# Optimization experiments

Hardware: AMD Instinct MI355X
Metric: run time of the kernel (lower is better)

## Reference

```python
import jax, jax.numpy as jnp
import numpy as np

NUM_EMBEDDINGS = 1024
EMBEDDING_DIM = 256
COMMITMENT_COST = 0.25


def setup_inputs() -> dict:
    key = jax.random.key(0)
    k1, k2 = jax.random.split(key)
    inputs = jax.random.normal(k1, (32, EMBEDDING_DIM, 32, 32), dtype=jnp.float32)
    # codebook init matches torch: uniform(-1/K, 1/K)
    weight = jax.random.uniform(
        k2, (NUM_EMBEDDINGS, EMBEDDING_DIM), dtype=jnp.float32,
        minval=-1.0 / NUM_EMBEDDINGS, maxval=1.0 / NUM_EMBEDDINGS)
    return {"inputs": inputs, "weight": weight}


def reference(inputs, weight):
    # inputs: [B, C, H, W] with C == EMBEDDING_DIM; weight: [K, D]
    x = jnp.transpose(inputs, (0, 2, 3, 1))            # [B, H, W, D]
    input_shape = x.shape
    flat = x.reshape(-1, EMBEDDING_DIM)                # [N, D]

    distances = (jnp.sum(flat * flat, axis=1, keepdims=True)
                 + jnp.sum(weight * weight, axis=1)
                 - 2.0 * (flat @ weight.T))
    encoding_indices = jnp.argmin(distances, axis=1)   # [N]
    encodings = jax.nn.one_hot(encoding_indices, NUM_EMBEDDINGS, dtype=jnp.float32)  # [N, K]

    # one_hot @ weight == gather; use gather for efficiency (same values)
    quantized = weight[encoding_indices].reshape(input_shape)  # [B, H, W, D]

    e_latent_loss = jnp.mean((jax.lax.stop_gradient(quantized) - x) ** 2)
    q_latent_loss = jnp.mean((quantized - jax.lax.stop_gradient(x)) ** 2)
    loss = q_latent_loss + COMMITMENT_COST * e_latent_loss

    # straight-through estimator
    quantized_st = x + jax.lax.stop_gradient(quantized - x)

    avg_probs = jnp.mean(encodings, axis=0)            # [K]
    perplexity = jnp.exp(-jnp.sum(avg_probs * jnp.log(avg_probs + 1e-10)))

    return (loss,
            jnp.transpose(quantized_st, (0, 3, 1, 2)),  # back to [B, C, H, W]
            perplexity,
            encodings)
```

## Files before the change

### kernel.cpp

```cpp
#include <hip/hip_runtime.h>
#include <hip/hip_bf16.h>

#define HWDIM 1024
#define DDIM 256
#define KCODES 1024
#define NROWS 32768
#define BSTRIDE (DDIM * HWDIM)
#define GUARD 1.5e-4f
#define APAD 520

typedef __attribute__((ext_vector_type(8))) short short8;
typedef __attribute__((ext_vector_type(4))) float f32x4;
typedef unsigned long long ull;


__device__ __forceinline__ unsigned short f2bf(float v) {
  __hip_bfloat16 b = __float2bfloat16(v);
  return *reinterpret_cast<unsigned short*>(&b);
}
__device__ __forceinline__ float bf2f(unsigned short u) {
  __hip_bfloat16 b;
  *reinterpret_cast<unsigned short*>(&b) = u;
  return __bfloat162float(b);
}
__device__ __forceinline__ ull pk(float d, int k) {
  unsigned ub = __float_as_uint(d);
  ub = (ub & 0x80000000u) ? ~ub : (ub | 0x80000000u);
  return ((ull)ub << 32) | (unsigned)k;
}
__device__ __forceinline__ float keyq(ull key) {
  unsigned ub = (unsigned)(key >> 32);
  unsigned orig = (ub & 0x80000000u) ? (ub & 0x7FFFFFFFu) : ~ub;
  return __uint_as_float(orig);
}
__device__ __forceinline__ float keyq32(unsigned ub) {
  unsigned orig = (ub & 0x80000000u) ? (ub & 0x7FFFFFFFu) : ~ub;
  return __uint_as_float(orig);
}

__device__ __forceinline__ float pair128_sq(const float* p, int stride) {
  float a[8];
#pragma unroll
  for (int j = 0; j < 8; ++j) { float v = p[j * stride]; a[j] = __fmul_rn(v, v); }
  for (int i = 8; i < 128; i += 8) {
#pragma unroll
    for (int j = 0; j < 8; ++j) {
      float v = p[(i + j) * stride];
      a[j] = __fadd_rn(a[j], __fmul_rn(v, v));
    }
  }
  float s01 = __fadd_rn(a[0], a[1]), s23 = __fadd_rn(a[2], a[3]);
  float s45 = __fadd_rn(a[4], a[5]), s67 = __fadd_rn(a[6], a[7]);
  return __fadd_rn(__fadd_rn(s01, s23), __fadd_rn(s45, s67));
}

__global__ __launch_bounds__(256) void k_prep(
    const float* __restrict__ w, float* __restrict__ wT, float* __restrict__ ss,
    int* __restrict__ hist, double* __restrict__ loss,
    int* __restrict__ wcount, int* __restrict__ pcount,
    unsigned short* __restrict__ wh8, unsigned short* __restrict__ wl8) {
  __shared__ float tile[64][65];
  const int t = threadIdx.x;
  int g = blockIdx.x * 256 + t;
  {
    int k = g >> 5, oct = g & 31;
    const float* p = w + k * DDIM + oct * 8;
    short8 hv, lv;
#pragma unroll
    for (int j = 0; j < 8; ++j) {
      float v = p[j];
      unsigned short h = f2bf(v);
      unsigned short l = f2bf(__fsub_rn(v, bf2f(h)));
      hv[j] = (short)h; lv[j] = (short)l;
    }
    *(short8*)&wh8[oct * 8192 + k * 8] = hv;
    *(short8*)&wl8[oct * 8192 + k * 8] = lv;
  }
  if (g < KCODES) {
    hist[g] = 0;
    const float* p = w + g * DDIM;
    ss[g] = __fadd_rn(pair128_sq(p, 1), pair128_sq(p + 128, 1));
  }
  if (g == 0) { *loss = 0.0; *wcount = 0; *pcount = 0; }
  if (blockIdx.x < 64) {
    const int k0 = (blockIdx.x & 15) * 64, d0 = (blockIdx.x >> 4) * 64;
    const int c = t & 63, r = t >> 6;
#pragma unroll
    for (int m = 0; m < 16; ++m)
      tile[r + m * 4][c] = w[(k0 + r + m * 4) * DDIM + d0 + c];
    __syncthreads();
#pragma unroll
    for (int m = 0; m < 16; ++m)
      wT[(size_t)(d0 + r + m * 4) * KCODES + k0 + c] = tile[c][r + m * 4];
  }
}

__global__ __launch_bounds__(256, 1) void k_argmfma(
    const float* __restrict__ in,
    const unsigned short* __restrict__ wh8, const unsigned short* __restrict__ wl8,
    const float* __restrict__ ss, unsigned* __restrict__ kkarr,
    int* __restrict__ wlist, int* __restrict__ wcount,
    int* __restrict__ plist, int* __restrict__ pcount) {
  __shared__ __align__(16) unsigned short Ah[32 * APAD];
  __shared__ __align__(16) unsigned short Al[32 * APAD];
  __shared__ __align__(16) float ss_l[1024];
  __shared__ ull best1[64], best2[64];
  __shared__ unsigned best3[64];

  const int t = threadIdx.x;
  const int n0 = blockIdx.x * 64;
  const int b = n0 >> 10, hw0 = n0 & 1023;

  const int wv = t >> 6, ln = t & 63;
  const int cw = wv * 64;
  const int l15 = ln & 15, quad = ln >> 4;

  {
    const int hw = t & 63, dg = t >> 6;
    const float* xp = in + b * BSTRIDE + hw0 + hw;
#pragma unroll
    for (int dd = 0; dd < 64; dd += 2) {
      int d = dg * 64 + dd;
      float f0 = __builtin_nontemporal_load(&xp[d * HWDIM]);
      float f1 = __builtin_nontemporal_load(&xp[(d + 1) * HWDIM]);
      unsigned short h0 = f2bf(f0);
      unsigned short l0 = f2bf(__fsub_rn(f0, bf2f(h0)));
      unsigned short h1 = f2bf(f1);
      unsigned short l1 = f2bf(__fsub_rn(f1, bf2f(h1)));
      int base = (d >> 3) * APAD + hw * 8 + (d & 7);
      *(unsigned*)&Ah[base] = (unsigned)h0 | ((unsigned)h1 << 16);
      *(unsigned*)&Al[base] = (unsigned)l0 | ((unsigned)l1 << 16);
    }
  }
  *(float4*)&ss_l[t * 4] = *(const float4*)&ss[t * 4];
  if (t < 64) { best1[t] = ~0ull; best2[t] = ~0ull; best3[t] = 0xFFFFFFFFu; }
  __syncthreads();

  ull rb1[16], rb2[16];
  unsigned rb3[16];
#pragma unroll
  for (int i = 0; i < 16; ++i) { rb1[i] = ~0ull; rb2[i] = ~0ull; rb3[i] = 0xFFFFFFFFu; }

  for (int kb = 0; kb < 4; ++kb) {
    const int cb = kb * 256 + cw;
    f32x4 acc[4][4];
#pragma unroll
    for (int rt = 0; rt < 4; ++rt)
#pragma unroll
      for (int ct = 0; ct < 4; ++ct) acc[rt][ct] = (f32x4){0.f, 0.f, 0.f, 0.f};

#pragma unroll
    for (int ki = 0; ki < 8; ++ki) {
      const int obase = ki * 4 + quad;
      short8 ah[4], al[4], bh[4], bl[4];
#pragma unroll
      for (int rt = 0; rt < 4; ++rt) {
        int row = rt * 16 + l15;
        ah[rt] = *(const short8*)&Ah[obase * APAD + row * 8];
        al[rt] = *(const short8*)&Al[obase * APAD + row * 8];
      }
#pragma unroll
      for (int ct = 0; ct < 4; ++ct) {
        int off = obase * 8192 + (cb + ct * 16 + l15) * 8;
        bh[ct] = *(const short8*)&wh8[off];
        bl[ct] = *(const short8*)&wl8[off];
      }
      __builtin_amdgcn_s_setprio(1);
#pragma unroll
      for (int rt = 0; rt < 4; ++rt)
#pragma unroll
        for (int ct = 0; ct < 4; ++ct) {
          acc[rt][ct] = __builtin_amdgcn_mfma_f32_16x16x32_bf16(ah[rt], bh[ct], acc[rt][ct], 0, 0, 0);
          acc[rt][ct] = __builtin_amdgcn_mfma_f32_16x16x32_bf16(ah[rt], bl[ct], acc[rt][ct], 0, 0, 0);
          acc[rt][ct] = __builtin_amdgcn_mfma_f32_16x16x32_bf16(al[rt], bh[ct], acc[rt][ct], 0, 0, 0);
        }
      __builtin_amdgcn_s_setprio(0);
    }

    float sv[4];
#pragma unroll
    for (int ct = 0; ct < 4; ++ct) sv[ct] = ss_l[cb + ct * 16 + l15];
#pragma unroll
    for (int rt = 0; rt < 4; ++rt)
#pragma unroll
      for (int reg = 0; reg < 4; ++reg) {
        int idx = rt * 4 + reg;
        ull b1 = rb1[idx], b2 = rb2[idx];
        unsigned b3 = rb3[idx];
#pragma unroll
        for (int ct = 0; ct < 4; ++ct) {
          float q = fmaf(-2.f, acc[rt][ct][reg], sv[ct]);
          ull key = pk(q, cb + ct * 16 + l15);
          unsigned k32 = (unsigned)(key >> 32);
          if (key < b1)      { b3 = (unsigned)(b2 >> 32); b2 = b1; b1 = key; }
          else if (key < b2) { b3 = (unsigned)(b2 >> 32); b2 = key; }
          else if (k32 < b3) { b3 = k32; }
        }
        rb1[idx] = b1; rb2[idx] = b2; rb3[idx] = b3;
      }
  }

#pragma unroll
  for (int rt = 0; rt < 4; ++rt)
#pragma unroll
    for (int reg = 0; reg < 4; ++reg)
      atomicMin(&best1[rt * 16 + quad * 4 + reg], rb1[rt * 4 + reg]);
  __syncthreads();
#pragma unroll
  for (int rt = 0; rt < 4; ++rt)
#pragma unroll
    for (int reg = 0; reg < 4; ++reg) {
      int row = rt * 16 + quad * 4 + reg;
      int idx = rt * 4 + reg;
      ull sub = (rb1[idx] == best1[row]) ? rb2[idx] : rb1[idx];
      atomicMin(&best2[row], sub);
    }
  __syncthreads();
#pragma unroll
  for (int rt = 0; rt < 4; ++rt)
#pragma unroll
    for (int reg = 0; reg < 4; ++reg) {
      int row = rt * 16 + quad * 4 + reg;
      int idx = rt * 4 + reg;
      ull b1 = best1[row], b2 = best2[row];
      unsigned c = (rb1[idx] != b1 && rb1[idx] != b2) ? (unsigned)(rb1[idx] >> 32)
                 : ((rb2[idx] != b1 && rb2[idx] != b2) ? (unsigned)(rb2[idx] >> 32)
                                                       : rb3[idx]);
      atomicMin(&best3[row], c);
    }
  __syncthreads();
  if (t < 64) {
    ull k1 = best1[t];
    kkarr[n0 + t] = (unsigned)(k1 & 0xFFFFFFFFull);
    float q1 = keyq(k1);
    if (!(keyq(best2[t]) - q1 > GUARD)) {
      if (keyq32(best3[t]) - q1 > GUARD) {
        int p = atomicAdd(pcount, 1);
        plist[p] = (n0 + t) | ((int)(best2[t] & 0xFFFFFFFFull) << 16);
      } else {
        int p = atomicAdd(wcount, 1);
        wlist[p] = n0 + t;
      }
    }
  }
}

__global__ __launch_bounds__(256) void k_fallback(
    const float* __restrict__ in, const float* __restrict__ w,
    const float* __restrict__ wT, const float* __restrict__ ss,
    const int* __restrict__ wlist, const int* __restrict__ wcount,
    const int* __restrict__ plist, const int* __restrict__ pcount,
    unsigned* __restrict__ kkarr) {
  __shared__ float xrow[256];
  __shared__ float rsh;
  __shared__ ull bmin;
  __shared__ ull pkeys[2];
  const int t = threadIdx.x;

  const int pc = *pcount;
  for (int i = blockIdx.x; i < pc; i += gridDim.x) {
    const int pe = plist[i];
    const int n = pe & 0xFFFF;
    const unsigned k2 = ((unsigned)pe) >> 16;
    const unsigned k1 = kkarr[n];
    const int b = n >> 10, hw = n & 1023;
    xrow[t] = in[b * BSTRIDE + t * HWDIM + hw];
    __syncthreads();
    if (t == 0) rsh = __fadd_rn(pair128_sq(xrow, 1), pair128_sq(xrow + 128, 1));
    __syncthreads();
    if (t < 2) {
      unsigned k = t ? k2 : k1;
      const float* wr = w + (size_t)k * DDIM;
      float m = 0.f;
      for (int d = 0; d < 256; ++d) m = fmaf(xrow[d], wr[d], m);
      float dist = fmaf(-2.f, m, __fadd_rn(rsh, ss[k]));
      pkeys[t] = pk(dist, (int)k);
    }
    __syncthreads();
    if (t == 0) {
      ull kmin = pkeys[0] < pkeys[1] ? pkeys[0] : pkeys[1];
      kkarr[n] = (unsigned)(kmin & 0xFFFFFFFFull);
    }
    __syncthreads();
  }

  const int cnt = *wcount;
  for (int i = blockIdx.x; i < cnt; i += gridDim.x) {
    const int n = wlist[i];
    const int b = n >> 10, hw = n & 1023;
    xrow[t] = in[b * BSTRIDE + t * HWDIM + hw];
    if (t == 0) bmin = ~0ull;
    __syncthreads();
    if (t == 0) rsh = __fadd_rn(pair128_sq(xrow, 1), pair128_sq(xrow + 128, 1));
    __syncthreads();
    float m[4] = {0.f, 0.f, 0.f, 0.f};
    for (int d = 0; d < 256; ++d) {
      float xv = xrow[d];
      const float* wd = wT + (size_t)d * KCODES + t;
      m[0] = fmaf(xv, wd[0], m[0]);
      m[1] = fmaf(xv, wd[256], m[1]);
      m[2] = fmaf(xv, wd[512], m[2]);
      m[3] = fmaf(xv, wd[768], m[3]);
    }
    ull lb = ~0ull;
#pragma unroll
    for (int j = 0; j < 4; ++j) {
      int k = t + j * 256;
      float dist = fmaf(-2.f, m[j], __fadd_rn(rsh, ss[k]));
      ull key = pk(dist, k);
      if (key < lb) lb = key;
    }
    atomicMin(&bmin, lb);
    __syncthreads();
    if (t == 0) kkarr[n] = (unsigned)(bmin & 0xFFFFFFFFull);
    __syncthreads();
  }
}

__global__ __launch_bounds__(256) void k_quantenc(
    const float* __restrict__ in, const float* __restrict__ w,
    const unsigned* __restrict__ kkarr, int* __restrict__ hist,
    float* __restrict__ enc, float* __restrict__ outq, double* __restrict__ loss) {
  __shared__ float wrow[64][65];
  __shared__ unsigned kk[64];
  __shared__ double red[256];

  const int t = threadIdx.x;
  const int q = blockIdx.x & 3;
  const int n0 = (blockIdx.x >> 2) * 64;
  const int dc = q * 64;
  const int c0 = q * 256;
  const int b = n0 >> 10, hw0 = n0 & 1023;

  if (t < 64) kk[t] = kkarr[n0 + t];
  __syncthreads();

  if (q == 0 && t < 64) atomicAdd(&hist[kk[t]], 1);

#pragma unroll 4
  for (int m = 0; m < 32; ++m) {
    int u = m * 256 + t;
    int r = u >> 7, c2 = u & 127;
    int cbase = c0 + c2 * 2;
    unsigned kr = kk[r];
    float2 v;
    v.x = (cbase == (int)kr) ? 1.0f : 0.0f;
    v.y = (cbase + 1 == (int)kr) ? 1.0f : 0.0f;
    *(float2*)&enc[(size_t)(n0 + r) * 1024 + cbase] = v;
  }

#pragma unroll
  for (int m = 0; m < 16; ++m) {
    int u = t + m * 256;
    int r = u >> 6, dd = u & 63;
    wrow[r][dd] = w[kk[r] * DDIM + dc + dd];
  }
  __syncthreads();

  const float* inb = in + b * BSTRIDE + hw0;
  float* outb = outq + b * BSTRIDE + hw0;
  const int hwl = t & 63, dl = t >> 6;
  double lsum = 0.0;
#pragma unroll
  for (int dd = 0; dd < 64; dd += 4) {
    int d = dc + dd + dl;
    float x = inb[d * HWDIM + hwl];
    float wv = wrow[hwl][dd + dl];
    float diff = __fsub_rn(wv, x);
    outb[d * HWDIM + hwl] = __fadd_rn(x, diff);
    lsum += (double)diff * (double)diff;
  }
  red[t] = lsum;
  __syncthreads();
  for (int s = 128; s > 0; s >>= 1) {
    if (t < s) red[t] += red[t + s];
    __syncthreads();
  }
  if (t == 0) atomicAdd(loss, red[0]);
}

__global__ void k_final(const int* __restrict__ hist, const double* __restrict__ loss,
                        float* __restrict__ out) {
  __shared__ double red[256];
  int t = threadIdx.x;
  double s = 0.0;
  for (int i = t; i < KCODES; i += 256) {
    double p = (double)hist[i] * (1.0 / 32768.0);
    s += p * log(p + 1e-10);
  }
  red[t] = s;
  __syncthreads();
  for (int st = 128; st > 0; st >>= 1) {
    if (t < st) red[t] += red[t + st];
    __syncthreads();
  }
  if (t == 0) {
    out[8388609] = (float)exp(-red[0]);
    double m = *loss / 8388608.0;
    out[0] = (float)(1.25 * m);
  }
}

extern "C" void kernel_launch(void* const* d_in, const int* in_sizes, int n_in,
                              void* d_out, int out_size, void* d_ws, size_t ws_size,
                              hipStream_t stream) {
  const float* in = (const float*)d_in[0];
  const float* w  = (const float*)d_in[1];
  float* out = (float*)d_out;

  char* wsb = (char*)d_ws;
  float*    wT     = (float*)   (wsb + 0);
  float*    ssp    = (float*)   (wsb + 1048576);
  unsigned* kkarr  = (unsigned*)(wsb + 1052672);
  int*      wlist  = (int*)     (wsb + 1183744);
  int*      hist   = (int*)     (wsb + 1314816);
  int*      plist  = (int*)     (wsb + 1318912);
  double*   loss   = (double*)  (wsb + 1449984);
  int*      wcount = (int*)     (wsb + 1449992);
  int*      pcount = (int*)     (wsb + 1449996);

  char* ob = (char*)d_out + 33554448;
  unsigned short* wh8 = (unsigned short*)(ob + 0);
  unsigned short* wl8 = (unsigned short*)(ob + 524288);
  float* encp = out + 8388610;

  k_prep<<<dim3(128), dim3(256), 0, stream>>>(w, wT, ssp, hist, loss, wcount, pcount, wh8, wl8);
  k_argmfma<<<dim3(512), dim3(256), 0, stream>>>(in, wh8, wl8, ssp, kkarr,
                                                 wlist, wcount, plist, pcount);
  k_fallback<<<dim3(1024), dim3(256), 0, stream>>>(in, w, wT, ssp, wlist, wcount,
                                                   plist, pcount, kkarr);
  k_quantenc<<<dim3(2048), dim3(256), 0, stream>>>(in, w, kkarr, hist, encp,
                                                   out + 1, loss);
  k_final<<<dim3(1), dim3(256), 0, stream>>>(hist, loss, out);
}
```

Baseline: 348.3 us.

## Split input bf16 hi/lo conversion into separate pre-pass kernel with MFMA-ready layout

Adds a k_split kernel that converts the fp32 NCHW input into bf16 hi/lo halves, stored in global scratch (inside the output buffer) in an octet-major layout matching the MFMA operand order. k_argmfma then loads these with contiguous 16-byte vector loads instead of doing strided fp32 loads and conversion itself, and drops the padded LDS layout. This is meant to cut the strided load latency from the single-block-per-CU GEMM kernel. In exchange it adds an extra kernel launch and a full write and re-read of about 32 MB of intermediate data, and the unpadded LDS layout may cause bank conflicts.

Result: slower. 365.1 us (+4.8%).

```diff
diff --git a/kernel.cpp b/kernel.cpp
--- a/kernel.cpp
+++ b/kernel.cpp
@@ -7,7 +7,6 @@
 #define NROWS 32768
 #define BSTRIDE (DDIM * HWDIM)
 #define GUARD 1.5e-4f
-#define APAD 520
 
 typedef __attribute__((ext_vector_type(8))) short short8;
 typedef __attribute__((ext_vector_type(4))) float f32x4;
@@ -95,41 +94,81 @@
   }
 }
 
+__global__ __launch_bounds__(256) void k_split(
+    const float* __restrict__ in,
+    unsigned short* __restrict__ AhG, unsigned short* __restrict__ AlG) {
+  __shared__ unsigned short sh[64 * 64];
+  __shared__ unsigned short sl[64 * 64];
+  const int t = threadIdx.x;
+  const int n0 = (blockIdx.x >> 2) * 64;
+  const int d0 = (blockIdx.x & 3) * 64;
+  const int b = n0 >> 10, hw0 = n0 & 1023;
+
+  {
+    const int hw = t & 63, dq = t >> 6;
+    const float* xp = in + b * BSTRIDE + hw0 + hw;
+#pragma unroll
+    for (int dd = 0; dd < 16; ++dd) {
+      int dl = dq * 16 + dd;
+      float v = xp[(d0 + dl) * HWDIM];
+      unsigned short h = f2bf(v);
+      unsigned short l = f2bf(__fsub_rn(v, bf2f(h)));
+      sh[dl * 64 + hw] = h;
+      sl[dl * 64 + hw] = l;
+    }
+  }
+  __syncthreads();
+  {
+    const int row = t & 63, oi = t >> 6;
+#pragma unroll
+    for (int it = 0; it < 2; ++it) {
+      int ol = oi + 4 * it;
+      int oct = (d0 >> 3) + ol;
+      short8 hv, lv;
+#pragma unroll
+      for (int j = 0; j < 8; ++j) {
+        hv[j] = (short)sh[(ol * 8 + j) * 64 + row];
+        lv[j] = (short)sl[(ol * 8 + j) * 64 + row];
+      }
+      size_t go = ((size_t)oct * NROWS + n0 + row) * 8;
+      *(short8*)&AhG[go] = hv;
+      *(short8*)&AlG[go] = lv;
+    }
+  }
+}
+
 __global__ __launch_bounds__(256, 1) void k_argmfma(
-    const float* __restrict__ in,
+    const unsigned short* __restrict__ AhG, const unsigned short* __restrict__ AlG,
     const unsigned short* __restrict__ wh8, const unsigned short* __restrict__ wl8,
     const float* __restrict__ ss, unsigned* __restrict__ kkarr,
     int* __restrict__ wlist, int* __restrict__ wcount,
     int* __restrict__ plist, int* __restrict__ pcount) {
-  __shared__ __align__(16) unsigned short Ah[32 * APAD];
-  __shared__ __align__(16) unsigned short Al[32 * APAD];
+  __shared__ __align__(16) unsigned short Ah[32 * 64 * 8];
+  __shared__ __align__(16) unsigned short Al[32 * 64 * 8];
   __shared__ __align__(16) float ss_l[1024];
   __shared__ ull best1[64], best2[64];
   __shared__ unsigned best3[64];
 
   const int t = threadIdx.x;
   const int n0 = blockIdx.x * 64;
-  const int b = n0 >> 10, hw0 = n0 & 1023;
-
   const int wv = t >> 6, ln = t & 63;
   const int cw = wv * 64;
   const int l15 = ln & 15, quad = ln >> 4;
 
   {
-    const int hw = t & 63, dg = t >> 6;
-    const float* xp = in + b * BSTRIDE + hw0 + hw;
-#pragma unroll
-    for (int dd = 0; dd < 64; dd += 2) {
-      int d = dg * 64 + dd;
-      float f0 = __builtin_nontemporal_load(&xp[d * HWDIM]);
-      float f1 = __builtin_nontemporal_load(&xp[(d + 1) * HWDIM]);
-      unsigned short h0 = f2bf(f0);
-      unsigned short l0 = f2bf(__fsub_rn(f0, bf2f(h0)));
-      unsigned short h1 = f2bf(f1);
-      unsigned short l1 = f2bf(__fsub_rn(f1, bf2f(h1)));
-      int base = (d >> 3) * APAD + hw * 8 + (d & 7);
-      *(unsigned*)&Ah[base] = (unsigned)h0 | ((unsigned)h1 << 16);
-      *(unsigned*)&Al[base] = (unsigned)l0 | ((unsigned)l1 << 16);
+    short8 th[8], tl[8];
+#pragma unroll
+    for (int i = 0; i < 8; ++i) {
+      int u = i * 256 + t;
+      size_t go = ((size_t)(u >> 6) * NROWS + n0 + (u & 63)) * 8;
+      th[i] = *(const short8*)&AhG[go];
+      tl[i] = *(const short8*)&AlG[go];
+    }
+#pragma unroll
+    for (int i = 0; i < 8; ++i) {
+      int u = i * 256 + t;
+      *(short8*)&Ah[u * 8] = th[i];
+      *(short8*)&Al[u * 8] = tl[i];
     }
   }
   *(float4*)&ss_l[t * 4] = *(const float4*)&ss[t * 4];
@@ -156,8 +195,8 @@
 #pragma unroll
       for (int rt = 0; rt < 4; ++rt) {
         int row = rt * 16 + l15;
-        ah[rt] = *(const short8*)&Ah[obase * APAD + row * 8];
-        al[rt] = *(const short8*)&Al[obase * APAD + row * 8];
+        ah[rt] = *(const short8*)&Ah[(obase * 64 + row) * 8];
+        al[rt] = *(const short8*)&Al[(obase * 64 + row) * 8];
       }
 #pragma unroll
       for (int ct = 0; ct < 4; ++ct) {
@@ -422,10 +461,13 @@
   char* ob = (char*)d_out + 33554448;
   unsigned short* wh8 = (unsigned short*)(ob + 0);
   unsigned short* wl8 = (unsigned short*)(ob + 524288);
+  unsigned short* AhG = (unsigned short*)(ob + 1048576);
+  unsigned short* AlG = (unsigned short*)(ob + 17825792);
   float* encp = out + 8388610;
 
   k_prep<<<dim3(128), dim3(256), 0, stream>>>(w, wT, ssp, hist, loss, wcount, pcount, wh8, wl8);
-  k_argmfma<<<dim3(512), dim3(256), 0, stream>>>(in, wh8, wl8, ssp, kkarr,
+  k_split<<<dim3(2048), dim3(256), 0, stream>>>(in, AhG, AlG);
+  k_argmfma<<<dim3(512), dim3(256), 0, stream>>>(AhG, AlG, wh8, wl8, ssp, kkarr,
                                                  wlist, wcount, plist, pcount);
   k_fallback<<<dim3(1024), dim3(256), 0, stream>>>(in, w, wT, ssp, wlist, wcount,
                                                    plist, pcount, kkarr);
```

## Stage codebook tiles in double-buffered LDS with register-resident A fragments

Applied to the files above, without the earlier changes.

The distance-argmin kernel now processes 128 rows per 512-thread block. Each wave keeps its 16-row A fragments in registers, and all waves share codebook B tiles staged through a double-buffered 128KB LDS region, prefetched from global memory one step ahead. Previously every wave loaded B fragments directly from global/L2 and re-read A from LDS. The aim is to reduce redundant global traffic and overlap loads with MFMA work. The cost is a sync per step, high LDS use that limits occupancy to one block per CU despite the launch bound of 2, and only 256 blocks.

Measured after the change: 314.9 us. 9.6% less time.

```diff
diff --git a/kernel.cpp b/kernel.cpp
--- a/kernel.cpp
+++ b/kernel.cpp
@@ -7,7 +7,6 @@
 #define NROWS 32768
 #define BSTRIDE (DDIM * HWDIM)
 #define GUARD 1.5e-4f
-#define APAD 520
 
 typedef __attribute__((ext_vector_type(8))) short short8;
 typedef __attribute__((ext_vector_type(4))) float f32x4;
@@ -95,28 +94,30 @@
   }
 }
 
-__global__ __launch_bounds__(256, 1) void k_argmfma(
+__global__ __launch_bounds__(512, 2) void k_argmfma(
     const float* __restrict__ in,
     const unsigned short* __restrict__ wh8, const unsigned short* __restrict__ wl8,
     const float* __restrict__ ss, unsigned* __restrict__ kkarr,
     int* __restrict__ wlist, int* __restrict__ wcount,
     int* __restrict__ plist, int* __restrict__ pcount) {
-  __shared__ __align__(16) unsigned short Ah[32 * APAD];
-  __shared__ __align__(16) unsigned short Al[32 * APAD];
+  __shared__ __align__(16) char smem[131072];
   __shared__ __align__(16) float ss_l[1024];
-  __shared__ ull best1[64], best2[64];
-  __shared__ unsigned best3[64];
+  __shared__ ull best1[128], best2[128];
+  __shared__ unsigned best3[128];
 
   const int t = threadIdx.x;
-  const int n0 = blockIdx.x * 64;
+  const int n0 = blockIdx.x * 128;
   const int b = n0 >> 10, hw0 = n0 & 1023;
 
   const int wv = t >> 6, ln = t & 63;
-  const int cw = wv * 64;
+  const int rw = wv * 16;
   const int l15 = ln & 15, quad = ln >> 4;
 
+  unsigned short* Ah = (unsigned short*)smem;
+  unsigned short* Al = (unsigned short*)(smem + 65536);
+
   {
-    const int hw = t & 63, dg = t >> 6;
+    const int hw = t & 127, dg = t >> 7;
     const float* xp = in + b * BSTRIDE + hw0 + hw;
 #pragma unroll
     for (int dd = 0; dd < 64; dd += 2) {
@@ -127,109 +128,146 @@
       unsigned short l0 = f2bf(__fsub_rn(f0, bf2f(h0)));
       unsigned short h1 = f2bf(f1);
       unsigned short l1 = f2bf(__fsub_rn(f1, bf2f(h1)));
-      int base = (d >> 3) * APAD + hw * 8 + (d & 7);
+      int base = ((d >> 3) * 128 + hw) * 8 + (d & 7);
       *(unsigned*)&Ah[base] = (unsigned)h0 | ((unsigned)h1 << 16);
       *(unsigned*)&Al[base] = (unsigned)l0 | ((unsigned)l1 << 16);
     }
   }
-  *(float4*)&ss_l[t * 4] = *(const float4*)&ss[t * 4];
-  if (t < 64) { best1[t] = ~0ull; best2[t] = ~0ull; best3[t] = 0xFFFFFFFFu; }
-  __syncthreads();
-
-  ull rb1[16], rb2[16];
-  unsigned rb3[16];
-#pragma unroll
-  for (int i = 0; i < 16; ++i) { rb1[i] = ~0ull; rb2[i] = ~0ull; rb3[i] = 0xFFFFFFFFu; }
-
-  for (int kb = 0; kb < 4; ++kb) {
-    const int cb = kb * 256 + cw;
-    f32x4 acc[4][4];
-#pragma unroll
-    for (int rt = 0; rt < 4; ++rt)
-#pragma unroll
-      for (int ct = 0; ct < 4; ++ct) acc[rt][ct] = (f32x4){0.f, 0.f, 0.f, 0.f};
+  *(float2*)&ss_l[t * 2] = *(const float2*)&ss[t * 2];
+  if (t < 128) { best1[t] = ~0ull; best2[t] = ~0ull; best3[t] = 0xFFFFFFFFu; }
+  __syncthreads();
+
+  short8 afh[8], afl[8];
+  {
+    const int row = rw + l15;
+#pragma unroll
+    for (int ki = 0; ki < 8; ++ki) {
+      int obase = ki * 4 + quad;
+      afh[ki] = *(const short8*)&Ah[(obase * 128 + row) * 8];
+      afl[ki] = *(const short8*)&Al[(obase * 128 + row) * 8];
+    }
+  }
+  short8 s0h[4], s0l[4];
+#pragma unroll
+  for (int j = 0; j < 4; ++j) {
+    int u = j * 512 + t;
+    int ob = u >> 6, c = u & 63;
+    s0h[j] = *(const short8*)&wh8[ob * 8192 + c * 8];
+    s0l[j] = *(const short8*)&wl8[ob * 8192 + c * 8];
+  }
+  __syncthreads();
+
+  {
+    unsigned short* Bh0 = (unsigned short*)smem;
+    unsigned short* Bl0 = (unsigned short*)(smem + 32768);
+#pragma unroll
+    for (int j = 0; j < 4; ++j) {
+      int u = j * 512 + t;
+      *(short8*)&Bh0[u * 8] = s0h[j];
+      *(short8*)&Bl0[u * 8] = s0l[j];
+    }
+  }
+  __syncthreads();
+
+  ull rb1[4], rb2[4];
+  unsigned rb3[4];
+#pragma unroll
+  for (int i = 0; i < 4; ++i) { rb1[i] = ~0ull; rb2[i] = ~0ull; rb3[i] = 0xFFFFFFFFu; }
+
+  int cur = 0;
+  for (int s = 0; s < 16; ++s) {
+    const int cb = s * 64;
+    short8 sh_[4], sl_[4];
+    if (s < 15) {
+      const int cb1 = cb + 64;
+#pragma unroll
+      for (int j = 0; j < 4; ++j) {
+        int u = j * 512 + t;
+        int ob = u >> 6, c = u & 63;
+        sh_[j] = *(const short8*)&wh8[ob * 8192 + (cb1 + c) * 8];
+        sl_[j] = *(const short8*)&wl8[ob * 8192 + (cb1 + c) * 8];
+      }
+    }
+
+    const unsigned short* Bh = (const unsigned short*)(smem + cur * 65536);
+    const unsigned short* Bl = (const unsigned short*)(smem + cur * 65536 + 32768);
+    f32x4 acc[4];
+#pragma unroll
+    for (int ct = 0; ct < 4; ++ct) acc[ct] = (f32x4){0.f, 0.f, 0.f, 0.f};
 
 #pragma unroll
     for (int ki = 0; ki < 8; ++ki) {
       const int obase = ki * 4 + quad;
-      short8 ah[4], al[4], bh[4], bl[4];
-#pragma unroll
-      for (int rt = 0; rt < 4; ++rt) {
-        int row = rt * 16 + l15;
-        ah[rt] = *(const short8*)&Ah[obase * APAD + row * 8];
-        al[rt] = *(const short8*)&Al[obase * APAD + row * 8];
-      }
+      short8 bh[4], bl[4];
 #pragma unroll
       for (int ct = 0; ct < 4; ++ct) {
-        int off = obase * 8192 + (cb + ct * 16 + l15) * 8;
-        bh[ct] = *(const short8*)&wh8[off];
-        bl[ct] = *(const short8*)&wl8[off];
-      }
-      __builtin_amdgcn_s_setprio(1);
-#pragma unroll
-      for (int rt = 0; rt < 4; ++rt)
-#pragma unroll
-        for (int ct = 0; ct < 4; ++ct) {
-          acc[rt][ct] = __builtin_amdgcn_mfma_f32_16x16x32_bf16(ah[rt], bh[ct], acc[rt][ct], 0, 0, 0);
-          acc[rt][ct] = __builtin_amdgcn_mfma_f32_16x16x32_bf16(ah[rt], bl[ct], acc[rt][ct], 0, 0, 0);
-          acc[rt][ct] = __builtin_amdgcn_mfma_f32_16x16x32_bf16(al[rt], bh[ct], acc[rt][ct], 0, 0, 0);
-        }
-      __builtin_amdgcn_s_setprio(0);
+        int uo = (obase * 64 + ct * 16 + l15) * 8;
+        bh[ct] = *(const short8*)&Bh[uo];
+        bl[ct] = *(const short8*)&Bl[uo];
+      }
+#pragma unroll
+      for (int ct = 0; ct < 4; ++ct) {
+        acc[ct] = __builtin_amdgcn_mfma_f32_16x16x32_bf16(afh[ki], bh[ct], acc[ct], 0, 0, 0);
+        acc[ct] = __builtin_amdgcn_mfma_f32_16x16x32_bf16(afh[ki], bl[ct], acc[ct], 0, 0, 0);
+        acc[ct] = __builtin_amdgcn_mfma_f32_16x16x32_bf16(afl[ki], bh[ct], acc[ct], 0, 0, 0);
+      }
     }
 
     float sv[4];
 #pragma unroll
     for (int ct = 0; ct < 4; ++ct) sv[ct] = ss_l[cb + ct * 16 + l15];
 #pragma unroll
-    for (int rt = 0; rt < 4; ++rt)
-#pragma unroll
-      for (int reg = 0; reg < 4; ++reg) {
-        int idx = rt * 4 + reg;
-        ull b1 = rb1[idx], b2 = rb2[idx];
-        unsigned b3 = rb3[idx];
-#pragma unroll
-        for (int ct = 0; ct < 4; ++ct) {
-          float q = fmaf(-2.f, acc[rt][ct][reg], sv[ct]);
-          ull key = pk(q, cb + ct * 16 + l15);
-          unsigned k32 = (unsigned)(key >> 32);
-          if (key < b1)      { b3 = (unsigned)(b2 >> 32); b2 = b1; b1 = key; }
-          else if (key < b2) { b3 = (unsigned)(b2 >> 32); b2 = key; }
-          else if (k32 < b3) { b3 = k32; }
-        }
-        rb1[idx] = b1; rb2[idx] = b2; rb3[idx] = b3;
-      }
-  }
-
-#pragma unroll
-  for (int rt = 0; rt < 4; ++rt)
-#pragma unroll
-    for (int reg = 0; reg < 4; ++reg)
-      atomicMin(&best1[rt * 16 + quad * 4 + reg], rb1[rt * 4 + reg]);
-  __syncthreads();
-#pragma unroll
-  for (int rt = 0; rt < 4; ++rt)
-#pragma unroll
     for (int reg = 0; reg < 4; ++reg) {
-      int row = rt * 16 + quad * 4 + reg;
-      int idx = rt * 4 + reg;
-      ull sub = (rb1[idx] == best1[row]) ? rb2[idx] : rb1[idx];
-      atomicMin(&best2[row], sub);
-    }
-  __syncthreads();
-#pragma unroll
-  for (int rt = 0; rt < 4; ++rt)
-#pragma unroll
-    for (int reg = 0; reg < 4; ++reg) {
-      int row = rt * 16 + quad * 4 + reg;
-      int idx = rt * 4 + reg;
-      ull b1 = best1[row], b2 = best2[row];
-      unsigned c = (rb1[idx] != b1 && rb1[idx] != b2) ? (unsigned)(rb1[idx] >> 32)
-                 : ((rb2[idx] != b1 && rb2[idx] != b2) ? (unsigned)(rb2[idx] >> 32)
-                                                       : rb3[idx]);
-      atomicMin(&best3[row], c);
-    }
-  __syncthreads();
-  if (t < 64) {
+      ull b1 = rb1[reg], b2 = rb2[reg];
+      unsigned b3 = rb3[reg];
+#pragma unroll
+      for (int ct = 0; ct < 4; ++ct) {
+        float q = fmaf(-2.f, acc[ct][reg], sv[ct]);
+        ull key = pk(q, cb + ct * 16 + l15);
+        unsigned k32 = (unsigned)(key >> 32);
+        if (key < b1)      { b3 = (unsigned)(b2 >> 32); b2 = b1; b1 = key; }
+        else if (key < b2) { b3 = (unsigned)(b2 >> 32); b2 = key; }
+        else if (k32 < b3) { b3 = k32; }
+      }
+      rb1[reg] = b1; rb2[reg] = b2; rb3[reg] = b3;
+    }
+
+    if (s < 15) {
+      unsigned short* BhN = (unsigned short*)(smem + (cur ^ 1) * 65536);
+      unsigned short* BlN = (unsigned short*)(smem + (cur ^ 1) * 65536 + 32768);
+#pragma unroll
+      for (int j = 0; j < 4; ++j) {
+        int u = j * 512 + t;
+        *(short8*)&BhN[u * 8] = sh_[j];
+        *(short8*)&BlN[u * 8] = sl_[j];
+      }
+    }
+    __syncthreads();
+    cur ^= 1;
+  }
+
+#pragma unroll
+  for (int reg = 0; reg < 4; ++reg)
+    atomicMin(&best1[rw + quad * 4 + reg], rb1[reg]);
+  __syncthreads();
+#pragma unroll
+  for (int reg = 0; reg < 4; ++reg) {
+    int row = rw + quad * 4 + reg;
+    ull sub = (rb1[reg] == best1[row]) ? rb2[reg] : rb1[reg];
+    atomicMin(&best2[row], sub);
+  }
+  __syncthreads();
+#pragma unroll
+  for (int reg = 0; reg < 4; ++reg) {
+    int row = rw + quad * 4 + reg;
+    ull b1 = best1[row], b2 = best2[row];
+    unsigned c = (rb1[reg] != b1 && rb1[reg] != b2) ? (unsigned)(rb1[reg] >> 32)
+               : ((rb2[reg] != b1 && rb2[reg] != b2) ? (unsigned)(rb2[reg] >> 32)
+                                                     : rb3[reg]);
+    atomicMin(&best3[row], c);
+  }
+  __syncthreads();
+  if (t < 128) {
     ull k1 = best1[t];
     kkarr[n0 + t] = (unsigned)(k1 & 0xFFFFFFFFull);
     float q1 = keyq(k1);
@@ -425,7 +463,7 @@
   float* encp = out + 8388610;
 
   k_prep<<<dim3(128), dim3(256), 0, stream>>>(w, wT, ssp, hist, loss, wcount, pcount, wh8, wl8);
-  k_argmfma<<<dim3(512), dim3(256), 0, stream>>>(in, wh8, wl8, ssp, kkarr,
+  k_argmfma<<<dim3(256), dim3(512), 0, stream>>>(in, wh8, wl8, ssp, kkarr,
                                                  wlist, wcount, plist, pcount);
   k_fallback<<<dim3(1024), dim3(256), 0, stream>>>(in, w, wT, ssp, wlist, wcount,
                                                    plist, pcount, kkarr);
```
